# Kernel optimization log

Hardware: AMD Instinct MI355X
Metric: run time of the kernel (lower is better)

The kernel has to match this reference:

```python
import jax, jax.numpy as jnp
import numpy as np

B, T, D = 4, 4096, 1024
C = 8.0  # RG_LRU constant c
LOGIT_LO = float(np.log(0.9 / 0.1))    # logit(0.9)
LOGIT_HI = float(np.log(0.999 / 0.001))  # logit(0.999)


def setup_inputs() -> dict:
    key = jax.random.key(0)
    ks = jax.random.split(key, 12)
    s = 1.0 / np.sqrt(D)
    z = lambda: jnp.zeros((D,), jnp.float32)
    return {
        "x": jax.random.normal(ks[0], (B, T, D), jnp.float32),
        "g1": jnp.ones((D,), jnp.float32),
        "g2": jnp.ones((D,), jnp.float32),
        # RecurrentBlock: shared linear, kernel-1 conv, output linear
        "W_lin": jax.random.normal(ks[1], (D, D), jnp.float32) * s, "b_lin": z(),
        "W_conv": jax.random.normal(ks[2], (D, D), jnp.float32) * s, "b_conv": z(),
        "W_lin2": jax.random.normal(ks[3], (D, D), jnp.float32) * s, "b_lin2": z(),
        # RG_LRU params
        "Wa": jax.random.normal(ks[4], (D, D), jnp.float32) * s, "ba": z(),
        "Wx": jax.random.normal(ks[5], (D, D), jnp.float32) * s, "bx": z(),
        "Lam": jax.random.uniform(ks[6], (D,), jnp.float32, LOGIT_LO, LOGIT_HI),
        # GatedMLPBlock
        "W1": jax.random.normal(ks[7], (D, D), jnp.float32) * s, "b1": z(),
        "W2": jax.random.normal(ks[8], (D, D), jnp.float32) * s, "b2": z(),
        "W3": jax.random.normal(ks[9], (D, D), jnp.float32) * s, "b3": z(),
    }


def rms_norm(x, g):
    # F.normalize(x, dim=-1) * sqrt(d) * g
    n = jnp.maximum(jnp.linalg.norm(x, axis=-1, keepdims=True), 1e-12)
    return (x / n) * (x.shape[-1] ** 0.5) * g


def rg_lru(x, Wa, ba, Wx, bx, Lam):
    # x: [B, T, D]
    rt = jax.nn.sigmoid(jnp.einsum('btd,hd->bth', x, Wa) + ba)
    it = jax.nn.sigmoid(jnp.einsum('btd,hd->bth', x, Wx) + bx)
    log_a = -jax.nn.softplus(-Lam)          # [D]
    a = jnp.exp(log_a * rt / C)             # [B, T, D]
    gated = jnp.sqrt(1.0 - a * a) * (it * x)

    def step(h, ag):
        at, gt = ag
        h = at * h + gt
        return h, h

    h0 = jnp.zeros((x.shape[0], x.shape[2]), x.dtype)
    _, hs = jax.lax.scan(step, h0, (jnp.swapaxes(a, 0, 1), jnp.swapaxes(gated, 0, 1)))
    return jnp.swapaxes(hs, 0, 1)           # [B, T, D]


def reference(x, g1, g2, W_lin, b_lin, W_conv, b_conv, W_lin2, b_lin2,
              Wa, ba, Wx, bx, Lam, W1, b1, W2, b2, W3, b3):
    residual = x
    xn = rms_norm(x, g1)

    # RecurrentBlock (note: same linear used for both branches, as in source)
    lin = xn @ W_lin.T + b_lin
    x_gel = jax.nn.gelu(lin, approximate=False)
    x_rg = lin @ W_conv.T + b_conv          # Conv1d kernel_size=1 == pointwise linear
    x_rg = rg_lru(x_rg, Wa, ba, Wx, bx, Lam)
    xr = (x_gel * x_rg) @ W_lin2.T + b_lin2

    residual = xr + residual
    xm = rms_norm(residual, g2)

    # GatedMLPBlock
    out = jax.nn.sigmoid(xm @ W1.T + b1)
    gate = jax.nn.gelu(out, approximate=False)
    combined = gate * (xm @ W2.T + b2)
    y = combined @ W3.T + b3
    return y + residual
```

## Files before the change

kernel.cpp:

```cpp
#include <hip/hip_runtime.h>
#include <cstdint>
#include <cstddef>

typedef unsigned short u16;
typedef __attribute__((ext_vector_type(8))) __bf16 bf16x8;
typedef __attribute__((ext_vector_type(4))) float f32x4;

#define DD 1024
#define MM 16384
#define NCH 64
#define CLEN 64
#define EPAD 136

__device__ __forceinline__ u16 f2b(float f) {
    uint32_t u = __float_as_uint(f);
    u += 0x7fffu + ((u >> 16) & 1u);
    return (u16)(u >> 16);
}
__device__ __forceinline__ float b2f(u16 v) {
    return __uint_as_float(((uint32_t)v) << 16);
}
__device__ __forceinline__ float sigmoid_f(float v) { return 1.f / (1.f + __expf(-v)); }
__device__ __forceinline__ float gelu_f(float v) {
    return 0.5f * v * (1.f + erff(v * 0.70710678118654752f));
}

__device__ __forceinline__ void swiz(int l, int& mt, int& nt) {
    const int g = l >> 6, r = l & 63;
    mt = g * 8 + (r & 7);
    nt = r >> 3;
}

template <int MODE>
__global__ __launch_bounds__(256, 2)
void gemm_bt(const u16* __restrict__ A, const u16* __restrict__ Bw,
             const float* __restrict__ bias, const float* __restrict__ auxf,
             u16* __restrict__ outb, float* __restrict__ outf)
{
    const int K = DD, N = DD;
    __shared__ __align__(16) u16 smem[8704];
    u16* const As = smem;
    u16* const Bs = smem + 4096;

    int mt, nt; swiz(blockIdx.x, mt, nt);
    const int m0 = mt * 128, n0 = nt * 128;
    const int tid = threadIdx.x;
    const int wave = tid >> 6, lane = tid & 63;
    const int wm = (wave >> 1) * 64, wn = (wave & 1) * 64;
    const int lr = lane & 15, lq = lane >> 4;

    const int trow = tid >> 2, tcol = tid & 3;
    const int kswz = (tcol ^ ((trow >> 1) & 3)) * 8;
    const u16* Ag = A + (size_t)(m0 + trow) * K + kswz;
    const u16* Bg = Bw + (size_t)(n0 + trow) * K + kswz;
    const int st = tid * 8;
    const int cs = (lq ^ ((lr >> 1) & 3)) * 8;

    f32x4 acc[4][4] = {};

    {
        const uint4 a0 = *(const uint4*)(Ag);
        const uint4 a1 = *(const uint4*)(Ag + (size_t)64 * K);
        const uint4 b0 = *(const uint4*)(Bg);
        const uint4 b1 = *(const uint4*)(Bg + (size_t)64 * K);
        *(uint4*)&As[st] = a0;
        *(uint4*)&As[st + 2048] = a1;
        *(uint4*)&Bs[st] = b0;
        *(uint4*)&Bs[st + 2048] = b1;
    }

    for (int k0 = 0; k0 < K; k0 += 32) {
        const int kn = k0 + 32;
        uint4 na0, na1, nb0, nb1;
        if (kn < K) {
            na0 = *(const uint4*)(Ag + kn);
            na1 = *(const uint4*)(Ag + (size_t)64 * K + kn);
            nb0 = *(const uint4*)(Bg + kn);
            nb1 = *(const uint4*)(Bg + (size_t)64 * K + kn);
        }
        asm volatile("s_waitcnt lgkmcnt(0)\ns_barrier" ::: "memory");

        bf16x8 av[4], bv[4];
#pragma unroll
        for (int i = 0; i < 4; i++)
            av[i] = *(const bf16x8*)&As[(wm + i * 16 + lr) * 32 + cs];
#pragma unroll
        for (int j = 0; j < 4; j++)
            bv[j] = *(const bf16x8*)&Bs[(wn + j * 16 + lr) * 32 + cs];
#pragma unroll
        for (int i = 0; i < 4; i++)
#pragma unroll
            for (int j = 0; j < 4; j++)
                acc[i][j] = __builtin_amdgcn_mfma_f32_16x16x32_bf16(
                    av[i], bv[j], acc[i][j], 0, 0, 0);

        asm volatile("s_barrier" ::: "memory");
        if (kn < K) {
            *(uint4*)&As[st] = na0;
            *(uint4*)&As[st + 2048] = na1;
            *(uint4*)&Bs[st] = nb0;
            *(uint4*)&Bs[st + 2048] = nb1;
        }
    }

    if constexpr (MODE == 2) {
#pragma unroll
        for (int i = 0; i < 4; i++) {
            const int mrow = m0 + wm + i * 16 + lq * 4;
#pragma unroll
            for (int j = 0; j < 4; j++) {
                const int ncol = n0 + wn + j * 16 + lr;
                const float bz = bias[ncol];
#pragma unroll
                for (int p = 0; p < 4; p++) {
                    const size_t idx = (size_t)(mrow + p) * N + ncol;
                    outf[idx] = acc[i][j][p] + bz + auxf[idx];
                }
            }
        }
    } else {
        for (int half = 0; half < 2; half++) {
            __syncthreads();
            if (wm == half * 64) {
#pragma unroll
                for (int i = 0; i < 4; i++)
#pragma unroll
                    for (int j = 0; j < 4; j++) {
                        const int col = wn + j * 16 + lr;
#pragma unroll
                        for (int p = 0; p < 4; p++)
                            smem[(i * 16 + lq * 4 + p) * EPAD + col] =
                                f2b(acc[i][j][p]);
                    }
            }
            __syncthreads();
#pragma unroll
            for (int t = 0; t < 4; t++) {
                const int f = t * 256 + tid;
                const int row = f >> 4, c8 = (f & 15) * 8;
                *(uint4*)&outb[(size_t)(m0 + half * 64 + row) * N + n0 + c8] =
                    *(const uint4*)&smem[row * EPAD + c8];
            }
        }
    }
}

template <int DMODE>
__global__ __launch_bounds__(256, 2)
void gemm_dual(const u16* __restrict__ A, const u16* __restrict__ B1,
               const u16* __restrict__ B2,
               const float* __restrict__ bias1, const float* __restrict__ bias2,
               u16* __restrict__ out1, u16* __restrict__ out2)
{
    const int K = DD, N = DD;
    __shared__ __align__(16) u16 smem[12288];
    u16* const As  = smem;
    u16* const B1s = smem + 4096;
    u16* const B2s = smem + 8192;

    int mt, nt; swiz(blockIdx.x, mt, nt);
    const int m0 = mt * 128, n0 = nt * 128;
    const int tid = threadIdx.x;
    const int wave = tid >> 6, lane = tid & 63;
    const int wm = (wave >> 1) * 64, wn = (wave & 1) * 64;
    const int lr = lane & 15, lq = lane >> 4;

    const int trow = tid >> 2, tcol = tid & 3;
    const int kswz = (tcol ^ ((trow >> 1) & 3)) * 8;
    const u16* Ag  = A  + (size_t)(m0 + trow) * K + kswz;
    const u16* B1g = B1 + (size_t)(n0 + trow) * K + kswz;
    const u16* B2g = B2 + (size_t)(n0 + trow) * K + kswz;
    const int st = tid * 8;
    const int cs = (lq ^ ((lr >> 1) & 3)) * 8;

    f32x4 acc1[4][4] = {}, acc2[4][4] = {};

    {
        const uint4 a0 = *(const uint4*)(Ag);
        const uint4 a1 = *(const uint4*)(Ag + (size_t)64 * K);
        const uint4 p0 = *(const uint4*)(B1g);
        const uint4 p1 = *(const uint4*)(B1g + (size_t)64 * K);
        const uint4 q0 = *(const uint4*)(B2g);
        const uint4 q1 = *(const uint4*)(B2g + (size_t)64 * K);
        *(uint4*)&As[st] = a0;
        *(uint4*)&As[st + 2048] = a1;
        *(uint4*)&B1s[st] = p0;
        *(uint4*)&B1s[st + 2048] = p1;
        *(uint4*)&B2s[st] = q0;
        *(uint4*)&B2s[st + 2048] = q1;
    }

    for (int k0 = 0; k0 < K; k0 += 32) {
        const int kn = k0 + 32;
        uint4 na0, na1, nb0, nb1, nc0, nc1;
        if (kn < K) {
            na0 = *(const uint4*)(Ag + kn);
            na1 = *(const uint4*)(Ag + (size_t)64 * K + kn);
            nb0 = *(const uint4*)(B1g + kn);
            nb1 = *(const uint4*)(B1g + (size_t)64 * K + kn);
            nc0 = *(const uint4*)(B2g + kn);
            nc1 = *(const uint4*)(B2g + (size_t)64 * K + kn);
        }
        asm volatile("s_waitcnt lgkmcnt(0)\ns_barrier" ::: "memory");

        bf16x8 av[4], bv1[4], bv2[4];
#pragma unroll
        for (int i = 0; i < 4; i++)
            av[i] = *(const bf16x8*)&As[(wm + i * 16 + lr) * 32 + cs];
#pragma unroll
        for (int j = 0; j < 4; j++) {
            bv1[j] = *(const bf16x8*)&B1s[(wn + j * 16 + lr) * 32 + cs];
            bv2[j] = *(const bf16x8*)&B2s[(wn + j * 16 + lr) * 32 + cs];
        }
#pragma unroll
        for (int i = 0; i < 4; i++)
#pragma unroll
            for (int j = 0; j < 4; j++) {
                acc1[i][j] = __builtin_amdgcn_mfma_f32_16x16x32_bf16(
                    av[i], bv1[j], acc1[i][j], 0, 0, 0);
                acc2[i][j] = __builtin_amdgcn_mfma_f32_16x16x32_bf16(
                    av[i], bv2[j], acc2[i][j], 0, 0, 0);
            }
        asm volatile("s_barrier" ::: "memory");
        if (kn < K) {
            *(uint4*)&As[st] = na0;
            *(uint4*)&As[st + 2048] = na1;
            *(uint4*)&B1s[st] = nb0;
            *(uint4*)&B1s[st + 2048] = nb1;
            *(uint4*)&B2s[st] = nc0;
            *(uint4*)&B2s[st + 2048] = nc1;
        }
    }

    if constexpr (DMODE == 0 || DMODE == 2) {
#pragma unroll
        for (int o = 0; o < 2; o++) {
            const float* bz = o ? bias2 : bias1;
            u16* op = o ? out2 : out1;
            for (int half = 0; half < 2; half++) {
                __syncthreads();
                if (wm == half * 64) {
#pragma unroll
                    for (int i = 0; i < 4; i++)
#pragma unroll
                        for (int j = 0; j < 4; j++) {
                            const int col = wn + j * 16 + lr;
                            const float bb = bz[n0 + col];
#pragma unroll
                            for (int p = 0; p < 4; p++) {
                                float v = (o ? acc2[i][j][p] : acc1[i][j][p]) + bb;
                                if constexpr (DMODE == 0) v = sigmoid_f(v);
                                smem[(i * 16 + lq * 4 + p) * EPAD + col] = f2b(v);
                            }
                        }
                }
                __syncthreads();
#pragma unroll
                for (int t = 0; t < 4; t++) {
                    const int f = t * 256 + tid;
                    const int row = f >> 4, c8 = (f & 15) * 8;
                    *(uint4*)&op[(size_t)(m0 + half * 64 + row) * N + n0 + c8] =
                        *(const uint4*)&smem[row * EPAD + c8];
                }
            }
        }
    } else {
        for (int half = 0; half < 2; half++) {
            __syncthreads();
            if (wm == half * 64) {
#pragma unroll
                for (int i = 0; i < 4; i++)
#pragma unroll
                    for (int j = 0; j < 4; j++) {
                        const int col = wn + j * 16 + lr;
                        const float bb1 = bias1[n0 + col];
                        const float bb2 = bias2[n0 + col];
#pragma unroll
                        for (int p = 0; p < 4; p++) {
                            const float g = gelu_f(sigmoid_f(acc1[i][j][p] + bb1));
                            smem[(i * 16 + lq * 4 + p) * EPAD + col] =
                                f2b(g * (acc2[i][j][p] + bb2));
                        }
                    }
            }
            __syncthreads();
#pragma unroll
            for (int t = 0; t < 4; t++) {
                const int f = t * 256 + tid;
                const int row = f >> 4, c8 = (f & 15) * 8;
                *(uint4*)&out1[(size_t)(m0 + half * 64 + row) * N + n0 + c8] =
                    *(const uint4*)&smem[row * EPAD + c8];
            }
        }
    }
}

__global__ __launch_bounds__(256)
void rmsnorm_k(const float* __restrict__ x, const float* __restrict__ g,
               u16* __restrict__ out)
{
    const int row = blockIdx.x;
    const int t = threadIdx.x;
    const float4 v = ((const float4*)(x + (size_t)row * DD))[t];
    float ss = v.x * v.x + v.y * v.y + v.z * v.z + v.w * v.w;
#pragma unroll
    for (int o = 32; o > 0; o >>= 1) ss += __shfl_down(ss, o, 64);
    __shared__ float wsum[4];
    if ((t & 63) == 0) wsum[t >> 6] = ss;
    __syncthreads();
    const float tot = wsum[0] + wsum[1] + wsum[2] + wsum[3];
    const float sc = 32.0f * rsqrtf(fmaxf(tot, 1e-24f));
    const float4 gv = ((const float4*)g)[t];
    ushort4 o4;
    o4.x = f2b(v.x * sc * gv.x);
    o4.y = f2b(v.y * sc * gv.y);
    o4.z = f2b(v.z * sc * gv.z);
    o4.w = f2b(v.w * sc * gv.w);
    ((ushort4*)(out + (size_t)row * DD))[t] = o4;
}

struct W8 { const float* s[8]; };
__global__ __launch_bounds__(256)
void conv_w8(W8 w, u16* __restrict__ out)
{
    const float* in = w.s[blockIdx.y];
    u16* o = out + (size_t)blockIdx.y * DD * DD;
    const int i = (blockIdx.x * 256 + threadIdx.x) * 4;
    const float4 v = *(const float4*)(in + i);
    ushort4 r;
    r.x = f2b(v.x); r.y = f2b(v.y); r.z = f2b(v.z); r.w = f2b(v.w);
    *(ushort4*)(o + i) = r;
}

__global__ __launch_bounds__(256)
void trans_k(const float* __restrict__ in, u16* __restrict__ out)
{
    __shared__ float tl[64][65];
    const int k0 = blockIdx.x * 64, d0 = blockIdx.y * 64;
    const int t = threadIdx.x, tr = t >> 4, tc = t & 15;
#pragma unroll
    for (int i = 0; i < 4; i++) {
        const int r = tr + i * 16;
        const float4 v = *(const float4*)(in + (size_t)(k0 + r) * DD + d0 + tc * 4);
        tl[r][tc * 4 + 0] = v.x; tl[r][tc * 4 + 1] = v.y;
        tl[r][tc * 4 + 2] = v.z; tl[r][tc * 4 + 3] = v.w;
    }
    __syncthreads();
#pragma unroll
    for (int i = 0; i < 4; i++) {
        const int r = tr + i * 16;
        ushort4 o;
        o.x = f2b(tl[tc * 4 + 0][r]);
        o.y = f2b(tl[tc * 4 + 1][r]);
        o.z = f2b(tl[tc * 4 + 2][r]);
        o.w = f2b(tl[tc * 4 + 3][r]);
        *(ushort4*)(out + (size_t)(d0 + r) * DD + k0 + tc * 4) = o;
    }
}

__global__ __launch_bounds__(256)
void bias_cl_k(const float* __restrict__ Wc, const float* __restrict__ bl,
               const float* __restrict__ bc, float* __restrict__ out)
{
    const int n = blockIdx.x * 4 + (threadIdx.x >> 6);
    const int lane = threadIdx.x & 63;
    float s = 0.f;
#pragma unroll
    for (int i = 0; i < 16; i++)
        s += Wc[(size_t)n * DD + lane + i * 64] * bl[lane + i * 64];
#pragma unroll
    for (int o = 32; o > 0; o >>= 1) s += __shfl_down(s, o, 64);
    if (lane == 0) out[n] = s + bc[n];
}

__global__ __launch_bounds__(256)
void scan_chunks(const u16* __restrict__ rt, const u16* __restrict__ it,
                 const u16* __restrict__ rg, const float* __restrict__ Lam,
                 float* __restrict__ P, float* __restrict__ Hl)
{
    const int d = blockIdx.x * 256 + threadIdx.x;
    const int c = blockIdx.y, b = blockIdx.z;
    const float k = -log1pf(__expf(-Lam[d])) * 0.125f;
    const size_t base = (((size_t)b * 4096) + (size_t)c * CLEN) * DD + d;
    float p = 1.f, h = 0.f;
#pragma unroll 4
    for (int t = 0; t < CLEN; t++) {
        const size_t ix = base + (size_t)t * DD;
        const float r = b2f(rt[ix]);
        const float i = b2f(it[ix]);
        const float xv = b2f(rg[ix]);
        const float a = __expf(k * r);
        const float g = sqrtf(fmaxf(1.f - a * a, 0.f)) * (i * xv);
        p *= a;
        h = fmaf(a, h, g);
    }
    const int o = (b * NCH + c) * DD + d;
    P[o] = p;
    Hl[o] = h;
}

__global__ __launch_bounds__(256)
void scan_carry(const float* __restrict__ P, const float* __restrict__ Hl,
                float* __restrict__ Cin)
{
    const int idx = blockIdx.x * 256 + threadIdx.x;
    const int b = idx >> 10, d = idx & 1023;
    float h = 0.f;
    for (int c = 0; c < NCH; c++) {
        const int o = (b * NCH + c) * DD + d;
        Cin[o] = h;
        h = fmaf(P[o], h, Hl[o]);
    }
}

__global__ __launch_bounds__(256)
void scan_apply(const u16* __restrict__ rt, const u16* __restrict__ it,
                const u16* __restrict__ rg, const u16* __restrict__ lin,
                const float* __restrict__ Lam, const float* __restrict__ Cin,
                u16* __restrict__ yin)
{
    const int d = blockIdx.x * 256 + threadIdx.x;
    const int c = blockIdx.y, b = blockIdx.z;
    const float k = -log1pf(__expf(-Lam[d])) * 0.125f;
    const size_t base = (((size_t)b * 4096) + (size_t)c * CLEN) * DD + d;
    float h = Cin[(b * NCH + c) * DD + d];
#pragma unroll 4
    for (int t = 0; t < CLEN; t++) {
        const size_t ix = base + (size_t)t * DD;
        const float r = b2f(rt[ix]);
        const float i = b2f(it[ix]);
        const float xv = b2f(rg[ix]);
        const float a = __expf(k * r);
        const float g = sqrtf(fmaxf(1.f - a * a, 0.f)) * (i * xv);
        h = fmaf(a, h, g);
        const float l = b2f(lin[ix]);
        yin[ix] = f2b(gelu_f(l) * h);
    }
}

extern "C" void kernel_launch(void* const* d_in, const int* in_sizes, int n_in,
                              void* d_out, int out_size, void* d_ws, size_t ws_size,
                              hipStream_t stream)
{
    const float* x      = (const float*)d_in[0];
    const float* g1     = (const float*)d_in[1];
    const float* g2     = (const float*)d_in[2];
    const float* W_lin  = (const float*)d_in[3];
    const float* b_lin  = (const float*)d_in[4];
    const float* W_conv = (const float*)d_in[5];
    const float* b_conv = (const float*)d_in[6];
    const float* W_lin2 = (const float*)d_in[7];
    const float* b_lin2 = (const float*)d_in[8];
    const float* Wa     = (const float*)d_in[9];
    const float* ba     = (const float*)d_in[10];
    const float* Wx     = (const float*)d_in[11];
    const float* bx     = (const float*)d_in[12];
    const float* Lam    = (const float*)d_in[13];
    const float* W1     = (const float*)d_in[14];
    const float* b1     = (const float*)d_in[15];
    const float* W2     = (const float*)d_in[16];
    const float* b2     = (const float*)d_in[17];
    const float* W3     = (const float*)d_in[18];
    const float* b3     = (const float*)d_in[19];
    float* out = (float*)d_out;

    char* p = (char*)d_ws;
    auto alloc = [&](size_t bytes) -> char* {
        char* q = p;
        p += (bytes + 255) & ~(size_t)255;
        return q;
    };
    const size_t MD = (size_t)MM * DD;
    u16* wball = (u16*)alloc((size_t)8 * DD * DD * 2);
    u16* wlinT = (u16*)alloc((size_t)DD * DD * 2);
    u16* Wcl   = (u16*)alloc((size_t)DD * DD * 2);
    float* bcl = (float*)alloc((size_t)DD * 4);
    u16* t0 = (u16*)alloc(MD * 2);
    u16* t1 = (u16*)alloc(MD * 2);
    u16* t2 = (u16*)alloc(MD * 2);
    u16* t3 = (u16*)alloc(MD * 2);
    u16* t4 = (u16*)alloc(MD * 2);
    float* res2 = (float*)alloc(MD * 4);
    float* P   = (float*)alloc((size_t)4 * NCH * DD * 4);
    float* Hl  = (float*)alloc((size_t)4 * NCH * DD * 4);
    float* Cin = (float*)alloc((size_t)4 * NCH * DD * 4);

    W8 w8;
    w8.s[0] = W_lin; w8.s[1] = W_conv; w8.s[2] = Wa; w8.s[3] = Wx;
    w8.s[4] = W_lin2; w8.s[5] = W1; w8.s[6] = W2; w8.s[7] = W3;
    conv_w8<<<dim3(DD * DD / 1024, 8), 256, 0, stream>>>(w8, wball);
    u16* wbf[8];
    for (int i = 0; i < 8; i++) wbf[i] = wball + (size_t)i * DD * DD;

    trans_k<<<dim3(16, 16), 256, 0, stream>>>(W_lin, wlinT);
    gemm_bt<6><<<64, 256, 0, stream>>>(wbf[1], wlinT, nullptr, nullptr, Wcl, nullptr);
    bias_cl_k<<<DD / 4, 256, 0, stream>>>(W_conv, b_lin, b_conv, bcl);

    const int gg = (MM / 128) * (DD / 128);
    const dim3 sg(DD / 256, NCH, 4);

    rmsnorm_k<<<MM, 256, 0, stream>>>(x, g1, t0);
    gemm_dual<2><<<gg, 256, 0, stream>>>(t0, wbf[0], Wcl, b_lin, bcl, t1, t2);
    gemm_dual<0><<<gg, 256, 0, stream>>>(t2, wbf[2], wbf[3], ba, bx, t0, t3);
    scan_chunks<<<sg, 256, 0, stream>>>(t0, t3, t2, Lam, P, Hl);
    scan_carry<<<4096 / 256, 256, 0, stream>>>(P, Hl, Cin);
    scan_apply<<<sg, 256, 0, stream>>>(t0, t3, t2, t1, Lam, Cin, t4);
    gemm_bt<2><<<gg, 256, 0, stream>>>(t4, wbf[4], b_lin2, x, nullptr, res2);
    rmsnorm_k<<<MM, 256, 0, stream>>>(res2, g2, t0);
    gemm_dual<1><<<gg, 256, 0, stream>>>(t0, wbf[5], wbf[6], b1, b2, t2, nullptr);
    gemm_bt<2><<<gg, 256, 0, stream>>>(t2, wbf[7], b3, res2, nullptr, out);
}
```

Before: 656.6 us.

## Load GEMM MFMA fragments directly from global memory, dropping LDS staging

Both GEMM kernels stop staging A/B tiles through shared memory. Each lane now loads its MFMA fragments straight from global memory into registers, double-buffered across two k-steps, and the per-iteration barriers are gone. The aim is to remove LDS write/read traffic and synchronisation stalls, and launch bounds are raised to 3 blocks per SM for the fp32-output mode. In exchange, each wave reads its own copy of the A and B tiles (now 2x redundant across waves instead of shared), which relies on L1/L2 to absorb duplicate fetches. Register pressure also rises with the doubled fragment buffers.

Result: slower. 1.092 ms (+66.3%).

```diff
diff --git a/kernel.cpp b/kernel.cpp
--- a/kernel.cpp
+++ b/kernel.cpp
@@ -32,15 +32,13 @@
 }
 
 template <int MODE>
-__global__ __launch_bounds__(256, 2)
+__global__ __launch_bounds__(256, (MODE == 2) ? 3 : 2)
 void gemm_bt(const u16* __restrict__ A, const u16* __restrict__ Bw,
              const float* __restrict__ bias, const float* __restrict__ auxf,
              u16* __restrict__ outb, float* __restrict__ outf)
 {
     const int K = DD, N = DD;
     __shared__ __align__(16) u16 smem[8704];
-    u16* const As = smem;
-    u16* const Bs = smem + 4096;
 
     int mt, nt; swiz(blockIdx.x, mt, nt);
     const int m0 = mt * 128, n0 = nt * 128;
@@ -49,59 +47,41 @@
     const int wm = (wave >> 1) * 64, wn = (wave & 1) * 64;
     const int lr = lane & 15, lq = lane >> 4;
 
-    const int trow = tid >> 2, tcol = tid & 3;
-    const int kswz = (tcol ^ ((trow >> 1) & 3)) * 8;
-    const u16* Ag = A + (size_t)(m0 + trow) * K + kswz;
-    const u16* Bg = Bw + (size_t)(n0 + trow) * K + kswz;
-    const int st = tid * 8;
-    const int cs = (lq ^ ((lr >> 1) & 3)) * 8;
-
+    const u16* Ap = A + (size_t)(m0 + wm + lr) * K + lq * 8;
+    const u16* Bp = Bw + (size_t)(n0 + wn + lr) * K + lq * 8;
+
+    bf16x8 a0[4], b0[4], a1[4], b1[4];
     f32x4 acc[4][4] = {};
 
-    {
-        const uint4 a0 = *(const uint4*)(Ag);
-        const uint4 a1 = *(const uint4*)(Ag + (size_t)64 * K);
-        const uint4 b0 = *(const uint4*)(Bg);
-        const uint4 b1 = *(const uint4*)(Bg + (size_t)64 * K);
-        *(uint4*)&As[st] = a0;
-        *(uint4*)&As[st + 2048] = a1;
-        *(uint4*)&Bs[st] = b0;
-        *(uint4*)&Bs[st + 2048] = b1;
-    }
-
-    for (int k0 = 0; k0 < K; k0 += 32) {
-        const int kn = k0 + 32;
-        uint4 na0, na1, nb0, nb1;
-        if (kn < K) {
-            na0 = *(const uint4*)(Ag + kn);
-            na1 = *(const uint4*)(Ag + (size_t)64 * K + kn);
-            nb0 = *(const uint4*)(Bg + kn);
-            nb1 = *(const uint4*)(Bg + (size_t)64 * K + kn);
-        }
-        asm volatile("s_waitcnt lgkmcnt(0)\ns_barrier" ::: "memory");
-
-        bf16x8 av[4], bv[4];
-#pragma unroll
-        for (int i = 0; i < 4; i++)
-            av[i] = *(const bf16x8*)&As[(wm + i * 16 + lr) * 32 + cs];
-#pragma unroll
-        for (int j = 0; j < 4; j++)
-            bv[j] = *(const bf16x8*)&Bs[(wn + j * 16 + lr) * 32 + cs];
-#pragma unroll
-        for (int i = 0; i < 4; i++)
-#pragma unroll
-            for (int j = 0; j < 4; j++)
-                acc[i][j] = __builtin_amdgcn_mfma_f32_16x16x32_bf16(
-                    av[i], bv[j], acc[i][j], 0, 0, 0);
-
-        asm volatile("s_barrier" ::: "memory");
-        if (kn < K) {
-            *(uint4*)&As[st] = na0;
-            *(uint4*)&As[st + 2048] = na1;
-            *(uint4*)&Bs[st] = nb0;
-            *(uint4*)&Bs[st + 2048] = nb1;
-        }
-    }
+#define LDF(av, bv, kk)                                                       \
+    {                                                                         \
+        _Pragma("unroll")                                                     \
+        for (int i = 0; i < 4; i++)                                           \
+            av[i] = *(const bf16x8*)(Ap + (size_t)i * 16 * K + (kk));         \
+        _Pragma("unroll")                                                     \
+        for (int j = 0; j < 4; j++)                                           \
+            bv[j] = *(const bf16x8*)(Bp + (size_t)j * 16 * K + (kk));         \
+    }
+#define MFM(av, bv)                                                           \
+    {                                                                         \
+        _Pragma("unroll")                                                     \
+        for (int i = 0; i < 4; i++)                                           \
+            _Pragma("unroll")                                                 \
+            for (int j = 0; j < 4; j++)                                       \
+                acc[i][j] = __builtin_amdgcn_mfma_f32_16x16x32_bf16(          \
+                    av[i], bv[j], acc[i][j], 0, 0, 0);                        \
+    }
+
+    LDF(a0, b0, 0);
+#pragma unroll 1
+    for (int k0 = 0; k0 < K; k0 += 64) {
+        LDF(a1, b1, k0 + 32);
+        MFM(a0, b0);
+        if (k0 + 64 < K) LDF(a0, b0, k0 + 64);
+        MFM(a1, b1);
+    }
+#undef LDF
+#undef MFM
 
     if constexpr (MODE == 2) {
 #pragma unroll
@@ -153,10 +133,7 @@
                u16* __restrict__ out1, u16* __restrict__ out2)
 {
     const int K = DD, N = DD;
-    __shared__ __align__(16) u16 smem[12288];
-    u16* const As  = smem;
-    u16* const B1s = smem + 4096;
-    u16* const B2s = smem + 8192;
+    __shared__ __align__(16) u16 smem[8704];
 
     int mt, nt; swiz(blockIdx.x, mt, nt);
     const int m0 = mt * 128, n0 = nt * 128;
@@ -165,72 +142,47 @@
     const int wm = (wave >> 1) * 64, wn = (wave & 1) * 64;
     const int lr = lane & 15, lq = lane >> 4;
 
-    const int trow = tid >> 2, tcol = tid & 3;
-    const int kswz = (tcol ^ ((trow >> 1) & 3)) * 8;
-    const u16* Ag  = A  + (size_t)(m0 + trow) * K + kswz;
-    const u16* B1g = B1 + (size_t)(n0 + trow) * K + kswz;
-    const u16* B2g = B2 + (size_t)(n0 + trow) * K + kswz;
-    const int st = tid * 8;
-    const int cs = (lq ^ ((lr >> 1) & 3)) * 8;
-
+    const u16* Ap  = A  + (size_t)(m0 + wm + lr) * K + lq * 8;
+    const u16* B1p = B1 + (size_t)(n0 + wn + lr) * K + lq * 8;
+    const u16* B2p = B2 + (size_t)(n0 + wn + lr) * K + lq * 8;
+
+    bf16x8 a0[4], p0[4], q0[4], a1[4], p1[4], q1[4];
     f32x4 acc1[4][4] = {}, acc2[4][4] = {};
 
-    {
-        const uint4 a0 = *(const uint4*)(Ag);
-        const uint4 a1 = *(const uint4*)(Ag + (size_t)64 * K);
-        const uint4 p0 = *(const uint4*)(B1g);
-        const uint4 p1 = *(const uint4*)(B1g + (size_t)64 * K);
-        const uint4 q0 = *(const uint4*)(B2g);
-        const uint4 q1 = *(const uint4*)(B2g + (size_t)64 * K);
-        *(uint4*)&As[st] = a0;
-        *(uint4*)&As[st + 2048] = a1;
-        *(uint4*)&B1s[st] = p0;
-        *(uint4*)&B1s[st + 2048] = p1;
-        *(uint4*)&B2s[st] = q0;
-        *(uint4*)&B2s[st + 2048] = q1;
-    }
-
-    for (int k0 = 0; k0 < K; k0 += 32) {
-        const int kn = k0 + 32;
-        uint4 na0, na1, nb0, nb1, nc0, nc1;
-        if (kn < K) {
-            na0 = *(const uint4*)(Ag + kn);
-            na1 = *(const uint4*)(Ag + (size_t)64 * K + kn);
-            nb0 = *(const uint4*)(B1g + kn);
-            nb1 = *(const uint4*)(B1g + (size_t)64 * K + kn);
-            nc0 = *(const uint4*)(B2g + kn);
-            nc1 = *(const uint4*)(B2g + (size_t)64 * K + kn);
-        }
-        asm volatile("s_waitcnt lgkmcnt(0)\ns_barrier" ::: "memory");
-
-        bf16x8 av[4], bv1[4], bv2[4];
-#pragma unroll
-        for (int i = 0; i < 4; i++)
-            av[i] = *(const bf16x8*)&As[(wm + i * 16 + lr) * 32 + cs];
-#pragma unroll
-        for (int j = 0; j < 4; j++) {
-            bv1[j] = *(const bf16x8*)&B1s[(wn + j * 16 + lr) * 32 + cs];
-            bv2[j] = *(const bf16x8*)&B2s[(wn + j * 16 + lr) * 32 + cs];
-        }
-#pragma unroll
-        for (int i = 0; i < 4; i++)
-#pragma unroll
-            for (int j = 0; j < 4; j++) {
-                acc1[i][j] = __builtin_amdgcn_mfma_f32_16x16x32_bf16(
-                    av[i], bv1[j], acc1[i][j], 0, 0, 0);
-                acc2[i][j] = __builtin_amdgcn_mfma_f32_16x16x32_bf16(
-                    av[i], bv2[j], acc2[i][j], 0, 0, 0);
-            }
-        asm volatile("s_barrier" ::: "memory");
-        if (kn < K) {
-            *(uint4*)&As[st] = na0;
-            *(uint4*)&As[st + 2048] = na1;
-            *(uint4*)&B1s[st] = nb0;
-            *(uint4*)&B1s[st + 2048] = nb1;
-            *(uint4*)&B2s[st] = nc0;
-            *(uint4*)&B2s[st + 2048] = nc1;
-        }
-    }
+#define LDF(av, pv, qv, kk)                                                   \
+    {                                                                         \
+        _Pragma("unroll")                                                     \
+        for (int i = 0; i < 4; i++)                                           \
+            av[i] = *(const bf16x8*)(Ap + (size_t)i * 16 * K + (kk));         \
+        _Pragma("unroll")                                                     \
+        for (int j = 0; j < 4; j++) {                                         \
+            pv[j] = *(const bf16x8*)(B1p + (size_t)j * 16 * K + (kk));        \
+            qv[j] = *(const bf16x8*)(B2p + (size_t)j * 16 * K + (kk));        \
+        }                                                                     \
+    }
+#define MFM(av, pv, qv)                                                       \
+    {                                                                         \
+        _Pragma("unroll")                                                     \
+        for (int i = 0; i < 4; i++)                                           \
+            _Pragma("unroll")                                                 \
+            for (int j = 0; j < 4; j++) {                                     \
+                acc1[i][j] = __builtin_amdgcn_mfma_f32_16x16x32_bf16(         \
+                    av[i], pv[j], acc1[i][j], 0, 0, 0);                       \
+                acc2[i][j] = __builtin_amdgcn_mfma_f32_16x16x32_bf16(         \
+                    av[i], qv[j], acc2[i][j], 0, 0, 0);                       \
+            }                                                                 \
+    }
+
+    LDF(a0, p0, q0, 0);
+#pragma unroll 1
+    for (int k0 = 0; k0 < K; k0 += 64) {
+        LDF(a1, p1, q1, k0 + 32);
+        MFM(a0, p0, q0);
+        if (k0 + 64 < K) LDF(a0, p0, q0, k0 + 64);
+        MFM(a1, p1, q1);
+    }
+#undef LDF
+#undef MFM
 
     if constexpr (DMODE == 0 || DMODE == 2) {
 #pragma unroll
```
